# Performance work log

Hardware: AMD Instinct MI355X
Metric: run time of the kernel (lower is better)

Reference implementation:

```python
import jax, jax.numpy as jnp
import numpy as np

B, VL, TL, KL = 2, 2048, 448, 64  # batch, vision_len, text_len, task_len
H, NH, D = 1024, 16, 64           # hidden, num_heads, head_dim


def _linear(x, w, b):
    # torch nn.Linear convention: w is [out, in]
    return x @ w.T + b


def _attn(q, k, v):
    # q: [b, ql, n, d], k/v: [b, kl, n, d] -> [b, ql, n, d]
    d = q.shape[-1]
    scores = jnp.einsum('bqnd,bknd->bnqk', q, k) / d  # note: /d, not /sqrt(d), as in source
    probs = jax.nn.softmax(scores, axis=-1)
    return jnp.einsum('bnqk,bknd->bqnd', probs, v)


def setup_inputs() -> dict:
    key = jax.random.key(0)
    ks = jax.random.split(key, 20)
    s = 0.02
    inp = {
        'vision_hidden_states': jax.random.normal(ks[0], (B, VL, H), jnp.float32),
        'text_hidden_states': jax.random.normal(ks[1], (B, TL, H), jnp.float32),
        'task_hidden_states': jax.random.normal(ks[2], (B, KL, H), jnp.float32),
        'wq0': jax.random.normal(ks[3], (H, H), jnp.float32) * s,
        'bq0': jnp.zeros((H,), jnp.float32),
        'wk0': jax.random.normal(ks[4], (H, H), jnp.float32) * s,
        'bk0': jnp.zeros((H,), jnp.float32),
        'wv0': jax.random.normal(ks[5], (H, H), jnp.float32) * s,
        'bv0': jnp.zeros((H,), jnp.float32),
        'wq1': jax.random.normal(ks[6], (D, D), jnp.float32) * s,
        'bq1': jnp.zeros((D,), jnp.float32),
        'wk1': jax.random.normal(ks[7], (D, D), jnp.float32) * s,
        'bk1': jnp.zeros((D,), jnp.float32),
        'wv1': jax.random.normal(ks[8], (D, D), jnp.float32) * s,
        'bv1': jnp.zeros((D,), jnp.float32),
        'wo': jax.random.normal(ks[9], (H, H), jnp.float32) * s,
        'bo': jnp.zeros((H,), jnp.float32),
    }
    return inp


def reference(vision_hidden_states, text_hidden_states, task_hidden_states,
              wq0, bq0, wk0, bk0, wv0, bv0,
              wq1, bq1, wk1, bk1, wv1, bv1, wo, bo):
    b, vl, h = vision_hidden_states.shape
    tl = text_hidden_states.shape[1]
    kl = task_hidden_states.shape[1]
    total = vl + tl + kl

    hs = jnp.concatenate([vision_hidden_states, text_hidden_states, task_hidden_states], axis=1)
    q0 = _linear(hs, wq0, bq0).reshape(b, total, NH, D)
    k0 = _linear(hs, wk0, bk0).reshape(b, total, NH, D)
    v0 = _linear(hs, wv0, bv0).reshape(b, total, NH, D)

    vq, tq, kq = q0[:, :vl], q0[:, vl:vl + tl], q0[:, vl + tl:]
    vk, tk, kk = k0[:, :vl], k0[:, vl:vl + tl], k0[:, vl + tl:]
    vv, tv = v0[:, :vl], v0[:, vl:vl + tl]
    kv = q0[:, vl + tl:]  # faithful to source bug: task_v comes from q0

    v2t = _attn(vq, tk, tv)  # vision attends to text: [b, vl, n, d]
    t2v = _attn(tq, vk, vv)  # text attends to vision: [b, tl, n, d]
    mid = jnp.concatenate([v2t, t2v], axis=1)  # [b, vl+tl, n, d]

    q1 = jnp.concatenate([kq, _linear(mid, wq1, bq1)], axis=1)
    k1 = jnp.concatenate([kk, _linear(mid, wk1, bk1)], axis=1)
    v1 = jnp.concatenate([kv, _linear(mid, wv1, bv1)], axis=1)

    out = _attn(q1, k1, v1).reshape(b, total, NH * D)
    return _linear(out, wo, bo)
```

## Files before the change

### kernel.cpp

```cpp
#include <hip/hip_runtime.h>
#include <math.h>

#define NB   2
#define VL   2048
#define TL   448
#define KL   64
#define TOT  2560
#define MIDL 2496
#define HDIM 1024
#define NHEAD 16
#define DHEAD 64

typedef __bf16 bf16x8 __attribute__((ext_vector_type(8)));
typedef float  f32x4  __attribute__((ext_vector_type(4)));
typedef unsigned short us8 __attribute__((ext_vector_type(8)));
typedef float  fl4    __attribute__((ext_vector_type(4)));
typedef unsigned int u32x2 __attribute__((ext_vector_type(2)));

__device__ __forceinline__ unsigned short f2bf(float f) {
    unsigned int u = __builtin_bit_cast(unsigned int, f);
    u += 0x7FFFu + ((u >> 16) & 1u);
    return (unsigned short)(u >> 16);
}
__device__ __forceinline__ float bf2f(unsigned short u) {
    unsigned int x = ((unsigned int)u) << 16;
    return __builtin_bit_cast(float, x);
}
__device__ __forceinline__ f32x4 mfma_bf16(bf16x8 a, bf16x8 b, f32x4 c) {
    return __builtin_amdgcn_mfma_f32_16x16x32_bf16(a, b, c, 0, 0, 0);
}
__device__ __forceinline__ bf16x8 ldb(const unsigned short* p) {
    return __builtin_bit_cast(bf16x8, *(const us8*)p);
}

__global__ __launch_bounds__(256) void k_cast_hs(
    const float* __restrict__ vis, const float* __restrict__ txt,
    const float* __restrict__ tsk, unsigned short* __restrict__ X)
{
    size_t idx = ((size_t)blockIdx.x * 256 + threadIdx.x) * 4;
    if (idx >= (size_t)NB * TOT * HDIM) return;
    size_t r = idx >> 10; int c = (int)(idx & 1023);
    int b = (int)(r / TOT), s = (int)(r % TOT);
    const float* src;
    if (s < VL)        src = vis + ((size_t)b * VL + s) * HDIM;
    else if (s < MIDL) src = txt + ((size_t)b * TL + (s - VL)) * HDIM;
    else               src = tsk + ((size_t)b * KL + (s - MIDL)) * HDIM;
    fl4 v = *(const fl4*)(src + c);
    X[idx + 0] = f2bf(v[0]); X[idx + 1] = f2bf(v[1]);
    X[idx + 2] = f2bf(v[2]); X[idx + 3] = f2bf(v[3]);
}

__global__ __launch_bounds__(256) void k_cast(
    const float* __restrict__ in, unsigned short* __restrict__ out, int n)
{
    int idx = (blockIdx.x * 256 + threadIdx.x) * 4;
    if (idx >= n) return;
    fl4 v = *(const fl4*)(in + idx);
    out[idx + 0] = f2bf(v[0]); out[idx + 1] = f2bf(v[1]);
    out[idx + 2] = f2bf(v[2]); out[idx + 3] = f2bf(v[3]);
}

template<bool BF16OUT>
__global__ __launch_bounds__(256) void k_gemm_bt(
    const unsigned short* __restrict__ A, const unsigned short* __restrict__ W,
    const float* __restrict__ bias, void* __restrict__ Cv,
    int M, int N, int K)
{
    __shared__ unsigned short As[128][40];
    __shared__ unsigned short Bs[128][40];
    const int row0 = blockIdx.x * 128, col0 = blockIdx.y * 128;
    const int t = threadIdx.x;
    const int lane = t & 63, wave = t >> 6;
    const int wr = wave >> 1, wc = wave & 1;
    const int lrow = lane & 15, lgrp = lane >> 4;

    f32x4 acc[4][4];
    #pragma unroll
    for (int m = 0; m < 4; ++m)
        #pragma unroll
        for (int n = 0; n < 4; ++n)
            acc[m][n] = (f32x4){0.f, 0.f, 0.f, 0.f};

    const int r = t >> 1, hc = (t & 1) * 16;
    const unsigned short* Ap = A + (size_t)(row0 + r) * K + hc;
    const unsigned short* Wp = W + (size_t)(col0 + r) * K + hc;

    for (int kk = 0; kk < K; kk += 32) {
        us8 a0 = *(const us8*)(Ap + kk);
        us8 a1 = *(const us8*)(Ap + kk + 8);
        us8 b0 = *(const us8*)(Wp + kk);
        us8 b1 = *(const us8*)(Wp + kk + 8);
        __syncthreads();
        *(us8*)&As[r][hc]     = a0;
        *(us8*)&As[r][hc + 8] = a1;
        *(us8*)&Bs[r][hc]     = b0;
        *(us8*)&Bs[r][hc + 8] = b1;
        __syncthreads();
        bf16x8 af[4], bfr[4];
        #pragma unroll
        for (int m = 0; m < 4; ++m) af[m]  = ldb(&As[wr*64 + m*16 + lrow][lgrp*8]);
        #pragma unroll
        for (int n = 0; n < 4; ++n) bfr[n] = ldb(&Bs[wc*64 + n*16 + lrow][lgrp*8]);
        #pragma unroll
        for (int m = 0; m < 4; ++m)
            #pragma unroll
            for (int n = 0; n < 4; ++n)
                acc[m][n] = mfma_bf16(af[m], bfr[n], acc[m][n]);
    }
    #pragma unroll
    for (int m = 0; m < 4; ++m) {
        #pragma unroll
        for (int n = 0; n < 4; ++n) {
            int col = col0 + wc*64 + n*16 + lrow;
            float bs = bias[col];
            #pragma unroll
            for (int q = 0; q < 4; ++q) {
                int row = row0 + wr*64 + m*16 + lgrp*4 + q;
                float v = acc[m][n][q] + bs;
                if (BF16OUT) ((unsigned short*)Cv)[(size_t)row * N + col] = f2bf(v);
                else         ((float*)Cv)[(size_t)row * N + col] = v;
            }
        }
    }
}

__global__ __launch_bounds__(256) void k_gemm_qkv(
    const unsigned short* __restrict__ A, const unsigned short* __restrict__ W,
    const float* __restrict__ b0, const float* __restrict__ b1,
    const float* __restrict__ b2,
    unsigned short* __restrict__ C0, unsigned short* __restrict__ C1,
    unsigned short* __restrict__ vT)
{
    __shared__ unsigned short As[128][40];
    __shared__ unsigned short Bs[128][40];
    const int row0 = blockIdx.x * 128, col0 = blockIdx.y * 128;
    const int t = threadIdx.x;
    const int lane = t & 63, wave = t >> 6;
    const int wr = wave >> 1, wc = wave & 1;
    const int lrow = lane & 15, lgrp = lane >> 4;

    f32x4 acc[4][4];
    #pragma unroll
    for (int m = 0; m < 4; ++m)
        #pragma unroll
        for (int n = 0; n < 4; ++n)
            acc[m][n] = (f32x4){0.f, 0.f, 0.f, 0.f};

    const int r = t >> 1, hc = (t & 1) * 16;
    const unsigned short* Ap = A + (size_t)(row0 + r) * HDIM + hc;
    const unsigned short* Wp = W + (size_t)(col0 + r) * HDIM + hc;

    for (int kk = 0; kk < HDIM; kk += 32) {
        us8 a0 = *(const us8*)(Ap + kk);
        us8 a1 = *(const us8*)(Ap + kk + 8);
        us8 b0v = *(const us8*)(Wp + kk);
        us8 b1v = *(const us8*)(Wp + kk + 8);
        __syncthreads();
        *(us8*)&As[r][hc]     = a0;
        *(us8*)&As[r][hc + 8] = a1;
        *(us8*)&Bs[r][hc]     = b0v;
        *(us8*)&Bs[r][hc + 8] = b1v;
        __syncthreads();
        bf16x8 af[4], bfr[4];
        #pragma unroll
        for (int m = 0; m < 4; ++m) af[m]  = ldb(&As[wr*64 + m*16 + lrow][lgrp*8]);
        #pragma unroll
        for (int n = 0; n < 4; ++n) bfr[n] = ldb(&Bs[wc*64 + n*16 + lrow][lgrp*8]);
        #pragma unroll
        for (int m = 0; m < 4; ++m)
            #pragma unroll
            for (int n = 0; n < 4; ++n)
                acc[m][n] = mfma_bf16(af[m], bfr[n], acc[m][n]);
    }
    const int plane = col0 >> 10;
    const int cl0 = col0 & 1023;
    if (plane < 2) {
        const float* bp = (plane == 0) ? b0 : b1;
        unsigned short* Cp = (plane == 0) ? C0 : C1;
        #pragma unroll
        for (int m = 0; m < 4; ++m)
            #pragma unroll
            for (int n = 0; n < 4; ++n) {
                int col = cl0 + wc*64 + n*16 + lrow;
                float bs = bp[col];
                #pragma unroll
                for (int q = 0; q < 4; ++q) {
                    int row = row0 + wr*64 + m*16 + lgrp*4 + q;
                    Cp[(size_t)row * HDIM + col] = f2bf(acc[m][n][q] + bs);
                }
            }
    } else {
        #pragma unroll
        for (int m = 0; m < 4; ++m)
            #pragma unroll
            for (int n = 0; n < 4; ++n) {
                int col = cl0 + wc*64 + n*16 + lrow;
                int hh = col >> 6, dd = col & 63;
                float bs = b2[col];
                int rowb = row0 + wr*64 + m*16 + lgrp*4;
                int bb = rowb / TOT, sq = rowb % TOT;
                unsigned short e0 = f2bf(acc[m][n][0] + bs);
                unsigned short e1 = f2bf(acc[m][n][1] + bs);
                unsigned short e2 = f2bf(acc[m][n][2] + bs);
                unsigned short e3 = f2bf(acc[m][n][3] + bs);
                u32x2 w;
                w[0] = (unsigned)e0 | ((unsigned)e1 << 16);
                w[1] = (unsigned)e2 | ((unsigned)e3 << 16);
                *(u32x2*)(vT + ((size_t)(bb*NHEAD + hh)*64 + dd)*TOT + sq) = w;
            }
    }
}

__global__ __launch_bounds__(256) void k_attn(
    const unsigned short* __restrict__ Qb, const unsigned short* __restrict__ Kb,
    const unsigned short* __restrict__ vT, unsigned short* __restrict__ Ob,
    int Lk, size_t q_bs, size_t k_bs, int v_seq0, size_t o_bs, float scale)
{
    __shared__ unsigned short QV[64 * 72];
    __shared__ unsigned short Ks[64][72];
    __shared__ unsigned short Pl[4][16][72];

    const int b = blockIdx.z, h = blockIdx.y, qb = blockIdx.x;
    const unsigned short* Q = Qb + (size_t)b * q_bs + h * 64;
    const unsigned short* K = Kb + (size_t)b * k_bs + h * 64;
    const unsigned short* V = vT + ((size_t)(b*NHEAD + h) * 64) * TOT + v_seq0;
    unsigned short*       O = Ob + (size_t)b * o_bs + h * 64;
    const int t = threadIdx.x;
    const int wave = t >> 6, lane = t & 63;
    const int lrow = lane & 15, lgrp = lane >> 4;
    const int q0r = qb * 64;

    #pragma unroll
    for (int i = 0; i < 2; ++i) {
        int c = t + i * 256, rr = c >> 3, off = (c & 7) * 8;
        *(us8*)&QV[rr*72 + off] = *(const us8*)(Q + (size_t)(q0r + rr) * HDIM + off);
    }
    __syncthreads();
    bf16x8 qf0 = ldb(&QV[(wave*16 + lrow)*72 + lgrp*8]);
    bf16x8 qf1 = ldb(&QV[(wave*16 + lrow)*72 + 32 + lgrp*8]);

    f32x4 oacc[4];
    #pragma unroll
    for (int d = 0; d < 4; ++d) oacc[d] = (f32x4){0.f, 0.f, 0.f, 0.f};
    float mr = -INFINITY;
    float lsum = 0.f;

    const int c0 = t,        rr0 = c0 >> 3, of0 = (c0 & 7) * 8;
    const int c1 = t + 256,  rr1 = c1 >> 3, of1 = (c1 & 7) * 8;
    const unsigned short* Kp0 = K + (size_t)rr0 * HDIM + of0;
    const unsigned short* Kp1 = K + (size_t)rr1 * HDIM + of1;
    const unsigned short* Vp0 = V + (size_t)rr0 * TOT + of0;
    const unsigned short* Vp1 = V + (size_t)rr1 * TOT + of1;

    const int nkt = Lk >> 6;
    us8 ka0 = *(const us8*)(Kp0);
    us8 ka1 = *(const us8*)(Kp1);
    us8 va0 = *(const us8*)(Vp0);
    us8 va1 = *(const us8*)(Vp1);

    for (int kt = 0; kt < nkt; ++kt) {
        __syncthreads();
        *(us8*)&Ks[rr0][of0] = ka0;
        *(us8*)&Ks[rr1][of1] = ka1;
        *(us8*)&QV[rr0*72 + of0] = va0;
        *(us8*)&QV[rr1*72 + of1] = va1;
        if (kt + 1 < nkt) {
            ka0 = *(const us8*)(Kp0 + (size_t)(kt+1) * 64 * HDIM);
            ka1 = *(const us8*)(Kp1 + (size_t)(kt+1) * 64 * HDIM);
            va0 = *(const us8*)(Vp0 + (kt+1) * 64);
            va1 = *(const us8*)(Vp1 + (kt+1) * 64);
        }
        __syncthreads();

        f32x4 s[4];
        #pragma unroll
        for (int nf = 0; nf < 4; ++nf) {
            bf16x8 kf0 = ldb(&Ks[nf*16 + lrow][lgrp*8]);
            bf16x8 kf1 = ldb(&Ks[nf*16 + lrow][32 + lgrp*8]);
            f32x4 z = (f32x4){0.f, 0.f, 0.f, 0.f};
            z = mfma_bf16(kf0, qf0, z);
            z = mfma_bf16(kf1, qf1, z);
            s[nf] = z * scale;
        }
        float mt = s[0][0];
        #pragma unroll
        for (int nf = 0; nf < 4; ++nf)
            #pragma unroll
            for (int rg = 0; rg < 4; ++rg)
                mt = fmaxf(mt, s[nf][rg]);
        mt = fmaxf(mt, __shfl_xor(mt, 16));
        mt = fmaxf(mt, __shfl_xor(mt, 32));
        float mn = fmaxf(mr, mt);
        float al = __expf(mr - mn);
        mr = mn;

        float rs = 0.f;
        #pragma unroll
        for (int nf = 0; nf < 4; ++nf) {
            unsigned short e0 = f2bf(__expf(s[nf][0] - mn));
            unsigned short e1 = f2bf(__expf(s[nf][1] - mn));
            unsigned short e2 = f2bf(__expf(s[nf][2] - mn));
            unsigned short e3 = f2bf(__expf(s[nf][3] - mn));
            rs += bf2f(e0) + bf2f(e1) + bf2f(e2) + bf2f(e3);
            u32x2 w;
            w[0] = (unsigned)e0 | ((unsigned)e1 << 16);
            w[1] = (unsigned)e2 | ((unsigned)e3 << 16);
            *(u32x2*)&Pl[wave][lrow][nf*16 + lgrp*4] = w;
        }
        rs += __shfl_xor(rs, 16);
        rs += __shfl_xor(rs, 32);
        lsum = lsum * al + rs;
        #pragma unroll
        for (int d = 0; d < 4; ++d) oacc[d] *= al;

        bf16x8 pb0 = ldb(&Pl[wave][lrow][lgrp*8]);
        bf16x8 pb1 = ldb(&Pl[wave][lrow][32 + lgrp*8]);
        #pragma unroll
        for (int df = 0; df < 4; ++df) {
            int d = df*16 + lrow;
            bf16x8 v0 = ldb(&QV[d*72 + lgrp*8]);
            bf16x8 v1 = ldb(&QV[d*72 + 32 + lgrp*8]);
            oacc[df] = mfma_bf16(v0, pb0, oacc[df]);
            oacc[df] = mfma_bf16(v1, pb1, oacc[df]);
        }
    }
    const float rcp = 1.0f / lsum;
    const int row = q0r + wave*16 + lrow;
    #pragma unroll
    for (int df = 0; df < 4; ++df) {
        unsigned short e0 = f2bf(oacc[df][0] * rcp);
        unsigned short e1 = f2bf(oacc[df][1] * rcp);
        unsigned short e2 = f2bf(oacc[df][2] * rcp);
        unsigned short e3 = f2bf(oacc[df][3] * rcp);
        u32x2 w;
        w[0] = (unsigned)e0 | ((unsigned)e1 << 16);
        w[1] = (unsigned)e2 | ((unsigned)e3 << 16);
        *(u32x2*)(O + (size_t)row * HDIM + df*16 + lgrp*4) = w;
    }
}

__global__ __launch_bounds__(256) void k_midlin(
    const unsigned short* __restrict__ mid,
    const unsigned short* __restrict__ wq, const unsigned short* __restrict__ wk,
    const unsigned short* __restrict__ wv,
    const float* __restrict__ bq, const float* __restrict__ bk,
    const float* __restrict__ bv,
    unsigned short* __restrict__ q1, unsigned short* __restrict__ k1,
    unsigned short* __restrict__ vT)
{
    __shared__ unsigned short As[128][72];
    const int r0 = blockIdx.x * 128, h = blockIdx.y;
    const int t = threadIdx.x;
    const int wave = t >> 6, lane = t & 63;
    const int lrow = lane & 15, lgrp = lane >> 4;

    #pragma unroll
    for (int i = 0; i < 4; ++i) {
        int c = t + i * 256, rr = c >> 3, off = (c & 7) * 8;
        *(us8*)&As[rr][off] = *(const us8*)(mid + (size_t)(r0 + rr) * HDIM + h*64 + off);
    }
    __syncthreads();
    bf16x8 af[2][2];
    #pragma unroll
    for (int m = 0; m < 2; ++m)
        #pragma unroll
        for (int kf = 0; kf < 2; ++kf)
            af[m][kf] = ldb(&As[wave*32 + m*16 + lrow][kf*32 + lgrp*8]);

    const unsigned short* ws[3] = {wq, wk, wv};
    const float* bs[3] = {bq, bk, bv};
    unsigned short* ds[2] = {q1, k1};
    #pragma unroll
    for (int o = 0; o < 3; ++o) {
        bf16x8 bfr[4][2];
        #pragma unroll
        for (int n = 0; n < 4; ++n)
            #pragma unroll
            for (int kf = 0; kf < 2; ++kf)
                bfr[n][kf] = __builtin_bit_cast(bf16x8,
                    *(const us8*)(ws[o] + (size_t)(n*16 + lrow) * 64 + kf*32 + lgrp*8));
        f32x4 acc[2][4];
        #pragma unroll
        for (int m = 0; m < 2; ++m)
            #pragma unroll
            for (int n = 0; n < 4; ++n) {
                f32x4 z = (f32x4){0.f, 0.f, 0.f, 0.f};
                z = mfma_bf16(af[m][0], bfr[n][0], z);
                z = mfma_bf16(af[m][1], bfr[n][1], z);
                acc[m][n] = z;
            }
        #pragma unroll
        for (int m = 0; m < 2; ++m)
            #pragma unroll
            for (int n = 0; n < 4; ++n) {
                float bb = bs[o][n*16 + lrow];
                if (o < 2) {
                    #pragma unroll
                    for (int q = 0; q < 4; ++q) {
                        int gr = r0 + wave*32 + m*16 + lgrp*4 + q;
                        int bi = gr / MIDL, sq = gr % MIDL;
                        size_t drow = (size_t)bi * TOT + 64 + sq;
                        ds[o][drow * HDIM + h*64 + n*16 + lrow] = f2bf(acc[m][n][q] + bb);
                    }
                } else {
                    int gr = r0 + wave*32 + m*16 + lgrp*4;
                    int bi = gr / MIDL, sq = gr % MIDL;
                    unsigned short e0 = f2bf(acc[m][n][0] + bb);
                    unsigned short e1 = f2bf(acc[m][n][1] + bb);
                    unsigned short e2 = f2bf(acc[m][n][2] + bb);
                    unsigned short e3 = f2bf(acc[m][n][3] + bb);
                    u32x2 w;
                    w[0] = (unsigned)e0 | ((unsigned)e1 << 16);
                    w[1] = (unsigned)e2 | ((unsigned)e3 << 16);
                    *(u32x2*)(vT + ((size_t)(bi*NHEAD + h)*64 + (n*16+lrow))*TOT
                              + 64 + sq) = w;
                }
            }
    }
}

__global__ __launch_bounds__(256) void k_copy_task(
    const unsigned short* __restrict__ q0, const unsigned short* __restrict__ k0,
    unsigned short* __restrict__ q1, unsigned short* __restrict__ k1,
    unsigned short* __restrict__ vT)
{
    int blk = blockIdx.x;
    int t = threadIdx.x;
    if (blk < 256) {
        int tensor = blk >> 7, rem = blk & 127;
        int b = rem >> 6, rr = rem & 63;
        const unsigned short* src = tensor ? k0 : q0;
        unsigned short* dst = tensor ? k1 : q1;
        size_t srow = (size_t)b * TOT + MIDL + rr;
        size_t drow = (size_t)b * TOT + rr;
        if (t < 128)
            ((us8*)(dst + drow * HDIM))[t] = ((const us8*)(src + srow * HDIM))[t];
    } else {
        int rem = blk - 256;
        int b = rem >> 4, h = rem & 15;
        const unsigned short* src = q0 + ((size_t)b * TOT + MIDL) * HDIM + h * 64;
        unsigned short* dst = vT + ((size_t)(b*NHEAD + h) * 64) * TOT;
        #pragma unroll
        for (int i = 0; i < 16; ++i) {
            int idx = t + i * 256;
            int r = idx & 63, d = idx >> 6;
            dst[(size_t)d * TOT + r] = src[(size_t)r * HDIM + d];
        }
    }
}

extern "C" void kernel_launch(void* const* d_in, const int* in_sizes, int n_in,
                              void* d_out, int out_size, void* d_ws, size_t ws_size,
                              hipStream_t stream)
{
    (void)in_sizes; (void)n_in; (void)out_size; (void)ws_size;
    const float* vis = (const float*)d_in[0];
    const float* txt = (const float*)d_in[1];
    const float* tsk = (const float*)d_in[2];
    const float* wq0 = (const float*)d_in[3];
    const float* bq0 = (const float*)d_in[4];
    const float* wk0 = (const float*)d_in[5];
    const float* bk0 = (const float*)d_in[6];
    const float* wv0 = (const float*)d_in[7];
    const float* bv0 = (const float*)d_in[8];
    const float* wq1 = (const float*)d_in[9];
    const float* bq1 = (const float*)d_in[10];
    const float* wk1 = (const float*)d_in[11];
    const float* bk1 = (const float*)d_in[12];
    const float* wv1 = (const float*)d_in[13];
    const float* bv1 = (const float*)d_in[14];
    const float* wo  = (const float*)d_in[15];
    const float* bo  = (const float*)d_in[16];

    char* ws = (char*)d_ws;
    size_t off = 0;
    auto carve = [&](size_t bytes) -> char* {
        char* p = ws + off;
        off += (bytes + 255) & ~(size_t)255;
        return p;
    };
    const size_t ELX = (size_t)NB * TOT * HDIM;
    unsigned short* X     = (unsigned short*)carve(ELX * 2);
    unsigned short* q0    = (unsigned short*)carve(ELX * 2);
    unsigned short* k0    = (unsigned short*)carve(ELX * 2);
    unsigned short* vT    = (unsigned short*)carve(ELX * 2);
    unsigned short* wqkvb = (unsigned short*)carve((size_t)3 * HDIM * HDIM * 2);
    unsigned short* wob   = (unsigned short*)carve((size_t)HDIM * HDIM * 2);
    unsigned short* wq1b  = (unsigned short*)carve(64 * 64 * 2);
    unsigned short* wk1b  = (unsigned short*)carve(64 * 64 * 2);
    unsigned short* wv1b  = (unsigned short*)carve(64 * 64 * 2);
    unsigned short* mid   = X;
    unsigned short* q1    = q0;
    unsigned short* k1    = k0;
    unsigned short* out2  = X;

    const float scale = 1.0f / 64.0f;

    k_cast_hs<<<5120, 256, 0, stream>>>(vis, txt, tsk, X);
    k_cast<<<1024, 256, 0, stream>>>(wq0, wqkvb,                 HDIM * HDIM);
    k_cast<<<1024, 256, 0, stream>>>(wk0, wqkvb + 1024*1024,     HDIM * HDIM);
    k_cast<<<1024, 256, 0, stream>>>(wv0, wqkvb + 2*1024*1024,   HDIM * HDIM);
    k_cast<<<1024, 256, 0, stream>>>(wo,  wob,  HDIM * HDIM);
    k_cast<<<4, 256, 0, stream>>>(wq1, wq1b, 64 * 64);
    k_cast<<<4, 256, 0, stream>>>(wk1, wk1b, 64 * 64);
    k_cast<<<4, 256, 0, stream>>>(wv1, wv1b, 64 * 64);

    k_gemm_qkv<<<dim3(40, 24), 256, 0, stream>>>(
        X, wqkvb, bq0, bk0, bv0, q0, k0, vT);

    k_attn<<<dim3(VL/64, NHEAD, NB), 256, 0, stream>>>(
        q0, k0 + (size_t)VL * HDIM, vT, mid,
        TL, (size_t)TOT * HDIM, (size_t)TOT * HDIM, VL, (size_t)MIDL * HDIM, scale);
    k_attn<<<dim3(TL/64, NHEAD, NB), 256, 0, stream>>>(
        q0 + (size_t)VL * HDIM, k0, vT, mid + (size_t)VL * HDIM,
        VL, (size_t)TOT * HDIM, (size_t)TOT * HDIM, 0, (size_t)MIDL * HDIM, scale);

    k_copy_task<<<288, 256, 0, stream>>>(q0, k0, q1, k1, vT);
    k_midlin<<<dim3(39, NHEAD), 256, 0, stream>>>(
        mid, wq1b, wk1b, wv1b, bq1, bk1, bv1, q1, k1, vT);

    k_attn<<<dim3(TOT/64, NHEAD, NB), 256, 0, stream>>>(
        q1, k1, vT, out2,
        TOT, (size_t)TOT * HDIM, (size_t)TOT * HDIM, 0, (size_t)TOT * HDIM, scale);

    k_gemm_bt<false><<<dim3(40, 8), 256, 0, stream>>>(out2, wob, bo, (float*)d_out,
                                                      NB*TOT, HDIM, HDIM);
}
```

Baseline: 411.0 us.

## Use exp2 with folded log2e, lazy softmax rescale, and packed bf16 conversions

Folds log2(e) into the attention scale so the softmax can use the raw v_exp_f32 (exp2) instruction instead of __expf. It skips the online-softmax rescale of the accumulators unless the running max grows by more than a threshold across the wave. It also replaces the manual round-to-nearest bf16 packing with the hardware v_cvt_pk_bf16_f32 instruction in attention and the V-transpose epilogues. The aim is to cut VALU work in the softmax and store paths. The trade-off is that the row sum is now accumulated from fp32 probabilities rather than the rounded bf16 values, and the lazy rescale allows unnormalized exponents up to 2^8.

```diff
diff --git a/kernel.cpp b/kernel.cpp
--- a/kernel.cpp
+++ b/kernel.cpp
@@ -22,15 +22,21 @@
     u += 0x7FFFu + ((u >> 16) & 1u);
     return (unsigned short)(u >> 16);
 }
-__device__ __forceinline__ float bf2f(unsigned short u) {
-    unsigned int x = ((unsigned int)u) << 16;
-    return __builtin_bit_cast(float, x);
-}
 __device__ __forceinline__ f32x4 mfma_bf16(bf16x8 a, bf16x8 b, f32x4 c) {
     return __builtin_amdgcn_mfma_f32_16x16x32_bf16(a, b, c, 0, 0, 0);
 }
 __device__ __forceinline__ bf16x8 ldb(const unsigned short* p) {
     return __builtin_bit_cast(bf16x8, *(const us8*)p);
+}
+__device__ __forceinline__ unsigned cvt_pk_bf16(float lo, float hi) {
+    unsigned r;
+    asm("v_cvt_pk_bf16_f32 %0, %1, %2" : "=v"(r) : "v"(lo), "v"(hi));
+    return r;
+}
+__device__ __forceinline__ float exp2_fast(float x) {
+    float r;
+    asm("v_exp_f32 %0, %1" : "=v"(r) : "v"(x));
+    return r;
 }
 
 __global__ __launch_bounds__(256) void k_cast_hs(
@@ -199,13 +205,9 @@
                 float bs = b2[col];
                 int rowb = row0 + wr*64 + m*16 + lgrp*4;
                 int bb = rowb / TOT, sq = rowb % TOT;
-                unsigned short e0 = f2bf(acc[m][n][0] + bs);
-                unsigned short e1 = f2bf(acc[m][n][1] + bs);
-                unsigned short e2 = f2bf(acc[m][n][2] + bs);
-                unsigned short e3 = f2bf(acc[m][n][3] + bs);
                 u32x2 w;
-                w[0] = (unsigned)e0 | ((unsigned)e1 << 16);
-                w[1] = (unsigned)e2 | ((unsigned)e3 << 16);
+                w[0] = cvt_pk_bf16(acc[m][n][0] + bs, acc[m][n][1] + bs);
+                w[1] = cvt_pk_bf16(acc[m][n][2] + bs, acc[m][n][3] + bs);
                 *(u32x2*)(vT + ((size_t)(bb*NHEAD + hh)*64 + dd)*TOT + sq) = w;
             }
     }
@@ -290,28 +292,31 @@
                 mt = fmaxf(mt, s[nf][rg]);
         mt = fmaxf(mt, __shfl_xor(mt, 16));
         mt = fmaxf(mt, __shfl_xor(mt, 32));
-        float mn = fmaxf(mr, mt);
-        float al = __expf(mr - mn);
-        mr = mn;
+        if (!__all(mt <= mr + 8.f)) {
+            float mnew = fmaxf(mr, mt);
+            float al = exp2_fast(mr - mnew);
+            mr = mnew;
+            lsum *= al;
+            #pragma unroll
+            for (int d = 0; d < 4; ++d) oacc[d] *= al;
+        }
 
         float rs = 0.f;
         #pragma unroll
         for (int nf = 0; nf < 4; ++nf) {
-            unsigned short e0 = f2bf(__expf(s[nf][0] - mn));
-            unsigned short e1 = f2bf(__expf(s[nf][1] - mn));
-            unsigned short e2 = f2bf(__expf(s[nf][2] - mn));
-            unsigned short e3 = f2bf(__expf(s[nf][3] - mn));
-            rs += bf2f(e0) + bf2f(e1) + bf2f(e2) + bf2f(e3);
+            float p0 = exp2_fast(s[nf][0] - mr);
+            float p1 = exp2_fast(s[nf][1] - mr);
+            float p2 = exp2_fast(s[nf][2] - mr);
+            float p3 = exp2_fast(s[nf][3] - mr);
+            rs += (p0 + p1) + (p2 + p3);
             u32x2 w;
-            w[0] = (unsigned)e0 | ((unsigned)e1 << 16);
-            w[1] = (unsigned)e2 | ((unsigned)e3 << 16);
+            w[0] = cvt_pk_bf16(p0, p1);
+            w[1] = cvt_pk_bf16(p2, p3);
             *(u32x2*)&Pl[wave][lrow][nf*16 + lgrp*4] = w;
         }
         rs += __shfl_xor(rs, 16);
         rs += __shfl_xor(rs, 32);
-        lsum = lsum * al + rs;
-        #pragma unroll
-        for (int d = 0; d < 4; ++d) oacc[d] *= al;
+        lsum += rs;
 
         bf16x8 pb0 = ldb(&Pl[wave][lrow][lgrp*8]);
         bf16x8 pb1 = ldb(&Pl[wave][lrow][32 + lgrp*8]);
@@ -328,13 +333,9 @@
     const int row = q0r + wave*16 + lrow;
     #pragma unroll
     for (int df = 0; df < 4; ++df) {
-        unsigned short e0 = f2bf(oacc[df][0] * rcp);
-        unsigned short e1 = f2bf(oacc[df][1] * rcp);
-        unsigned short e2 = f2bf(oacc[df][2] * rcp);
-        unsigned short e3 = f2bf(oacc[df][3] * rcp);
         u32x2 w;
-        w[0] = (unsigned)e0 | ((unsigned)e1 << 16);
-        w[1] = (unsigned)e2 | ((unsigned)e3 << 16);
+        w[0] = cvt_pk_bf16(oacc[df][0] * rcp, oacc[df][1] * rcp);
+        w[1] = cvt_pk_bf16(oacc[df][2] * rcp, oacc[df][3] * rcp);
         *(u32x2*)(O + (size_t)row * HDIM + df*16 + lgrp*4) = w;
     }
 }
@@ -405,13 +406,9 @@
                 } else {
                     int gr = r0 + wave*32 + m*16 + lgrp*4;
                     int bi = gr / MIDL, sq = gr % MIDL;
-                    unsigned short e0 = f2bf(acc[m][n][0] + bb);
-                    unsigned short e1 = f2bf(acc[m][n][1] + bb);
-                    unsigned short e2 = f2bf(acc[m][n][2] + bb);
-                    unsigned short e3 = f2bf(acc[m][n][3] + bb);
                     u32x2 w;
-                    w[0] = (unsigned)e0 | ((unsigned)e1 << 16);
-                    w[1] = (unsigned)e2 | ((unsigned)e3 << 16);
+                    w[0] = cvt_pk_bf16(acc[m][n][0] + bb, acc[m][n][1] + bb);
+                    w[1] = cvt_pk_bf16(acc[m][n][2] + bb, acc[m][n][3] + bb);
                     *(u32x2*)(vT + ((size_t)(bi*NHEAD + h)*64 + (n*16+lrow))*TOT
                               + 64 + sq) = w;
                 }
@@ -494,7 +491,7 @@
     unsigned short* k1    = k0;
     unsigned short* out2  = X;
 
-    const float scale = 1.0f / 64.0f;
+    const float scale = 1.44269504088896341f / 64.0f;
 
     k_cast_hs<<<5120, 256, 0, stream>>>(vis, txt, tsk, X);
     k_cast<<<1024, 256, 0, stream>>>(wq0, wqkvb,                 HDIM * HDIM);
```

After: 389.5 us. 1.05x faster.
